# Kernel optimization log

Measured on AMD Instinct MI355X. Metric: run time of the kernel, lower is better.

Reference implementation:

```python
import jax, jax.numpy as jnp
import numpy as np

EPS = 1e-5

def conv(x, w, b, stride, pad):
    y = jax.lax.conv_general_dilated(x, w, (stride, stride), [(pad, pad), (pad, pad)],
                                     dimension_numbers=('NCHW', 'OIHW', 'NCHW'))
    return y + b[None, :, None, None]

def inorm(x):
    # InstanceNorm2d, affine=False, eps=1e-5, biased variance over H,W
    m = x.mean(axis=(2, 3), keepdims=True)
    v = ((x - m) ** 2).mean(axis=(2, 3), keepdims=True)
    return (x - m) * jax.lax.rsqrt(v + EPS)

def setup_inputs() -> dict:
    key = jax.random.key(0)
    ks = jax.random.split(key, 24)
    B = 64
    x = jax.random.normal(ks[0], (B, 5, 256, 192), dtype=jnp.float32)
    chans = [(5, 8), (8, 16), (16, 32), (32, 64), (64, 128), (128, 256)]
    params = {'x': x}
    for i, (ci, co) in enumerate(chans):
        fan = ci * 16
        params[f'w{i}'] = jax.random.normal(ks[1 + 2 * i], (co, ci, 4, 4), jnp.float32) / np.sqrt(fan)
        params[f'b{i}'] = jnp.zeros((co,), jnp.float32)
    for i in (6, 7):
        params[f'w{i}'] = jax.random.normal(ks[1 + 2 * i], (256, 256, 3, 3), jnp.float32) / np.sqrt(256 * 9)
        params[f'b{i}'] = jnp.zeros((256,), jnp.float32)
    params['fc1_w'] = jax.random.normal(ks[20], (128, 512), jnp.float32) / np.sqrt(512)
    params['fc1_b'] = jnp.zeros((128,), jnp.float32)
    # fc2: weight zeroed at init in original; use small random for a nontrivial baseline
    params['fc2_w'] = jax.random.normal(ks[21], (50, 128), jnp.float32) * 0.01
    lin = np.linspace(-0.9, 0.9, 5, dtype=np.float32)
    yy, xx = np.meshgrid(lin, lin, indexing='ij')
    tcp = np.stack([xx.ravel(), yy.ravel()], axis=1)  # [25,2]
    params['fc2_b'] = jnp.asarray(np.arctanh(tcp).reshape(-1))  # [50]
    return params

def reference(x, w0, b0, w1, b1, w2, b2, w3, b3, w4, b4, w5, b5, w6, b6, w7, b7,
              fc1_w, fc1_b, fc2_w, fc2_b):
    B = x.shape[0]
    # block 0: conv -> relu -> instance_norm
    h = inorm(jax.nn.relu(conv(x, w0, b0, 2, 1)))
    # blocks 1..5: conv -> instance_norm -> relu, stride 2
    for w, b in ((w1, b1), (w2, b2), (w3, b3), (w4, b4), (w5, b5)):
        h = jax.nn.relu(inorm(conv(h, w, b, 2, 1)))
    # two 3x3 stride-1 blocks
    for w, b in ((w6, b6), (w7, b7)):
        h = jax.nn.relu(inorm(conv(h, w, b, 1, 1)))
    # maxpool 2x2 stride 2
    h = jax.lax.reduce_window(h, -jnp.inf, jax.lax.max, (1, 1, 2, 2), (1, 1, 2, 2), 'VALID')
    h = h.reshape(B, -1)  # [B,512]
    h = jax.nn.relu(h @ fc1_w.T + fc1_b)
    # F.dropout in eval mode = identity (reference is deterministic)
    pts = jnp.tanh(h @ fc2_w.T + fc2_b)  # [B,50]
    coor = pts.reshape(B, -1, 2)          # [B,25,2]
    grid = coor.reshape(B, 5, 5, 2)       # [B, row j, col i, (x,y)]

    # get_row: squared diffs along i, then abs second difference; stack order (j outer, i inner)
    d_row = (grid[:, :, 1:] - grid[:, :, :-1]) ** 2            # [B,5,4,2]
    row = jnp.abs(d_row[:, :, 1:] - d_row[:, :, :-1]).reshape(B, 15, 2)
    # get_col: same along j; stack order (i outer, j inner)
    gT = jnp.swapaxes(grid, 1, 2)                              # [B, i, j, 2]
    d_col = (gT[:, :, 1:] - gT[:, :, :-1]) ** 2
    col = jnp.abs(d_col[:, :, 1:] - d_col[:, :, :-1]).reshape(B, 15, 2)

    # grad_row / grad_col: curvature cross-product terms, BATCH ELEMENT 0 ONLY (as in original)
    def curv(g):  # g: [5,5,2], triplets along axis 1
        p0, p1, p2 = g[:, :-2], g[:, 1:-1], g[:, 2:]
        x0, y0 = p0[..., 0], p0[..., 1]
        x1, y1 = p1[..., 0], p1[..., 1]
        x2, y2 = p2[..., 0], p2[..., 1]
        return jnp.abs((y1 - y0) * (x1 - x2) - (y1 - y2) * (x1 - x0))  # [5,3]

    g0 = grid[0]
    rg_loss = jnp.maximum(curv(g0).sum(), 0.02)
    cg_loss = jnp.maximum(curv(jnp.swapaxes(g0, 0, 1)).sum(), 0.02)

    rx_loss = jnp.maximum(0.08, row[:, :, 0]).mean()
    ry_loss = jnp.maximum(0.08, row[:, :, 1]).mean()
    cx_loss = jnp.maximum(0.08, col[:, :, 0]).mean()
    cy_loss = jnp.maximum(0.08, col[:, :, 1]).mean()
    return (coor, rx_loss, ry_loss, cx_loss, cy_loss, rg_loss, cg_loss)
```

## Files before the change

### kernel.cpp

```cpp
#include <hip/hip_runtime.h>
#include <hip/hip_bf16.h>
#include <math.h>

#define EPS 1e-5f

__global__ __launch_bounds__(256) void conv0(const float* __restrict__ in,
                                             const float* __restrict__ w,
                                             const float* __restrict__ bias,
                                             float* __restrict__ out)
{
    __shared__ float sW[5 * 8 * 16];
    __shared__ float sB[8];
    int t   = threadIdx.x;
    int n   = blockIdx.x / 24;
    int pxb = blockIdx.x % 24;
    for (int i = t; i < 640; i += 256) {
        int ci = i / 128;
        int r  = i % 128;
        int co = r / 16;
        int k  = r % 16;
        sW[i] = w[((size_t)co * 5 + ci) * 16 + k];
    }
    if (t < 8) sB[t] = bias[t];
    __syncthreads();

    int px0 = (pxb * 256 + t) * 2;
    int oh  = px0 / 96;
    int ow0 = px0 % 96;
    int ih0 = oh * 2 - 1;
    int iwq = ow0 * 2;

    float acc[8][2];
#pragma unroll
    for (int j = 0; j < 8; ++j) { acc[j][0] = sB[j]; acc[j][1] = sB[j]; }

    const float* ib = in + (size_t)n * 5 * 256 * 192;
#pragma unroll 1
    for (int ci = 0; ci < 5; ++ci) {
        const float* plane = ib + (size_t)ci * 256 * 192;
#pragma unroll
        for (int kh = 0; kh < 4; ++kh) {
            int ih = ih0 + kh;
            float p[6];
            if ((unsigned)ih < 256u) {
                const float* row = plane + (size_t)ih * 192;
                float4 q = *(const float4*)(row + iwq);
                p[1] = q.x; p[2] = q.y; p[3] = q.z; p[4] = q.w;
                p[0] = (iwq >= 1)      ? row[iwq - 1] : 0.f;
                p[5] = (iwq + 4 < 192) ? row[iwq + 4] : 0.f;
            } else {
#pragma unroll
                for (int k2 = 0; k2 < 6; ++k2) p[k2] = 0.f;
            }
#pragma unroll
            for (int j = 0; j < 8; ++j) {
                const float4 wv = *(const float4*)(sW + (ci * 8 + j) * 16 + kh * 4);
                acc[j][0] = fmaf(p[0], wv.x, acc[j][0]);
                acc[j][0] = fmaf(p[1], wv.y, acc[j][0]);
                acc[j][0] = fmaf(p[2], wv.z, acc[j][0]);
                acc[j][0] = fmaf(p[3], wv.w, acc[j][0]);
                acc[j][1] = fmaf(p[2], wv.x, acc[j][1]);
                acc[j][1] = fmaf(p[3], wv.y, acc[j][1]);
                acc[j][1] = fmaf(p[4], wv.z, acc[j][1]);
                acc[j][1] = fmaf(p[5], wv.w, acc[j][1]);
            }
        }
    }
    float* ob = out + (size_t)n * 8 * 12288 + px0;
#pragma unroll
    for (int j = 0; j < 8; ++j) {
        float2 v;
        v.x = fmaxf(acc[j][0], 0.f);
        v.y = fmaxf(acc[j][1], 0.f);
        *(float2*)(ob + (size_t)j * 12288) = v;
    }
}

template<int CIN, int CPT>
__global__ void conv42(const float* __restrict__ in, const float* __restrict__ w,
                       const float* __restrict__ bias, float* __restrict__ out,
                       int N, int H, int W, int COUT, int OH, int OW, int relu)
{
    const int NPX = OH * OW;
    const int PXB = NPX / blockDim.x;
    const int NCG = COUT / CPT;

    int bx  = blockIdx.x;
    int pxb = bx % PXB;
    int cg  = (bx / PXB) % NCG;
    int n   = bx / (PXB * NCG);
    int tid = threadIdx.x;

    __shared__ float sW[CPT * CIN * 16];
    for (int i = tid; i < CPT * CIN * 16; i += blockDim.x) {
        int ci = i / (CPT * 16);
        int r  = i % (CPT * 16);
        int j  = r / 16;
        int k  = r % 16;
        sW[i] = w[((size_t)(cg * CPT + j) * CIN + ci) * 16 + k];
    }
    __syncthreads();

    int px = pxb * blockDim.x + tid;
    int oh = px / OW, ow = px % OW;
    int ih0 = oh * 2 - 1, iw0 = ow * 2 - 1;

    float acc[CPT];
#pragma unroll
    for (int j = 0; j < CPT; ++j) acc[j] = bias[cg * CPT + j];

    const float* ib = in + (size_t)n * CIN * H * W;
#pragma unroll 1
    for (int ci = 0; ci < CIN; ++ci) {
        float p[16];
        const float* plane = ib + (size_t)ci * H * W;
#pragma unroll
        for (int kh = 0; kh < 4; ++kh) {
            int ih = ih0 + kh;
            bool vr = (unsigned)ih < (unsigned)H;
            const float* row = plane + (size_t)ih * W;
#pragma unroll
            for (int kw = 0; kw < 4; ++kw) {
                int iw = iw0 + kw;
                bool v = vr && ((unsigned)iw < (unsigned)W);
                p[kh * 4 + kw] = v ? row[iw] : 0.f;
            }
        }
        const float* wp = sW + ci * CPT * 16;
#pragma unroll
        for (int j = 0; j < CPT; ++j) {
            const float* wj = wp + j * 16;
#pragma unroll
            for (int k = 0; k < 16; ++k) acc[j] = fmaf(p[k], wj[k], acc[j]);
        }
    }

#pragma unroll
    for (int j = 0; j < CPT; ++j) {
        float v = acc[j];
        if (relu) v = fmaxf(v, 0.f);
        out[((size_t)(n * COUT + cg * CPT + j) * OH + oh) * OW + ow] = v;
    }
}

__global__ __launch_bounds__(192) void conv_l3s(const float* __restrict__ in,
                                                const float* __restrict__ w,
                                                float* __restrict__ pbuf)
{
    __shared__ float sW[8 * 8 * 16];
    int t  = threadIdx.x;
    int b  = blockIdx.x;
    int cg = b & 7;
    int s  = (b >> 3) & 3;
    int n  = b >> 5;
    for (int i = t; i < 1024; i += 192) {
        int ci = i >> 7;
        int r  = i & 127;
        int j  = r >> 4;
        int k  = r & 15;
        sW[i] = w[((size_t)(cg * 8 + j) * 32 + s * 8 + ci) * 16 + k];
    }
    __syncthreads();

    int oh = t / 12, ow = t % 12;
    int ih0 = oh * 2 - 1, iw0 = ow * 2 - 1;
    float acc[8];
#pragma unroll
    for (int j = 0; j < 8; ++j) acc[j] = 0.f;

    const float* ib = in + ((size_t)n * 32 + s * 8) * 768;
#pragma unroll 1
    for (int ci = 0; ci < 8; ++ci) {
        const float* plane = ib + ci * 768;
        float p[16];
#pragma unroll
        for (int kh = 0; kh < 4; ++kh) {
            int ih = ih0 + kh;
            bool vr = (unsigned)ih < 32u;
#pragma unroll
            for (int kw = 0; kw < 4; ++kw) {
                int iw = iw0 + kw;
                bool v = vr && ((unsigned)iw < 24u);
                p[kh * 4 + kw] = v ? plane[ih * 24 + iw] : 0.f;
            }
        }
        const float* wp = sW + ci * 128;
#pragma unroll
        for (int j = 0; j < 8; ++j) {
#pragma unroll
            for (int k = 0; k < 16; ++k)
                acc[j] = fmaf(p[k], wp[j * 16 + k], acc[j]);
        }
    }
    float* pb = pbuf + (((size_t)s * 64 + n) * 64 + cg * 8) * 192 + t;
#pragma unroll
    for (int j = 0; j < 8; ++j) pb[j * 192] = acc[j];
}

__global__ __launch_bounds__(256) void reduce_norm_l3T(const float* __restrict__ pbuf,
                                                       float* __restrict__ dst_t)
{
    int gid  = blockIdx.x * blockDim.x + threadIdx.x;
    int wv   = gid >> 6;
    int lane = gid & 63;
    int n  = wv >> 6;
    int co = wv & 63;
    float tv[3];
#pragma unroll
    for (int k = 0; k < 3; ++k) {
        int i = lane + k * 64;
        float sum = 0.f;
#pragma unroll
        for (int s = 0; s < 4; ++s)
            sum += pbuf[((size_t)s * 4096 + wv) * 192 + i];
        tv[k] = sum;
    }
    float s1 = tv[0] + tv[1] + tv[2];
    float s2 = tv[0]*tv[0] + tv[1]*tv[1] + tv[2]*tv[2];
    for (int m = 32; m >= 1; m >>= 1) {
        s1 += __shfl_xor(s1, m);
        s2 += __shfl_xor(s2, m);
    }
    float mean = s1 * (1.f / 192.f);
    float var  = s2 * (1.f / 192.f) - mean * mean;
    float r = rsqrtf(var + EPS);
#pragma unroll
    for (int k = 0; k < 3; ++k) {
        int i = lane + k * 64;
        float y = fmaxf((tv[k] - mean) * r, 0.f);
        dst_t[((size_t)co * 192 + i) * 64 + n] = y;
    }
}

template<int TPB, int VPT>
__global__ void inorm_blockv(float* __restrict__ data, int relu)
{
    const int HW = TPB * VPT * 4;
    float4* p = (float4*)(data + (size_t)blockIdx.x * HW);
    float4 v[VPT];
    float s = 0.f, q = 0.f;
#pragma unroll
    for (int k = 0; k < VPT; ++k) {
        v[k] = p[threadIdx.x + k * TPB];
        s += v[k].x + v[k].y + v[k].z + v[k].w;
        q += v[k].x*v[k].x + v[k].y*v[k].y + v[k].z*v[k].z + v[k].w*v[k].w;
    }
    for (int m2 = 32; m2 >= 1; m2 >>= 1) {
        s += __shfl_xor(s, m2);
        q += __shfl_xor(q, m2);
    }
    __shared__ float ss[TPB / 64], sq[TPB / 64], sm[2];
    int wave = threadIdx.x >> 6, lane = threadIdx.x & 63;
    if (lane == 0) { ss[wave] = s; sq[wave] = q; }
    __syncthreads();
    if (threadIdx.x == 0) {
        float a = 0.f, b2 = 0.f;
#pragma unroll
        for (int k = 0; k < TPB / 64; ++k) { a += ss[k]; b2 += sq[k]; }
        float mm = a / (float)HW;
        float vv = b2 / (float)HW - mm * mm;
        sm[0] = mm; sm[1] = rsqrtf(vv + EPS);
    }
    __syncthreads();
    float m = sm[0], r = sm[1];
#pragma unroll
    for (int k = 0; k < VPT; ++k) {
        float4 y;
        y.x = (v[k].x - m) * r; y.y = (v[k].y - m) * r;
        y.z = (v[k].z - m) * r; y.w = (v[k].w - m) * r;
        if (relu) {
            y.x = fmaxf(y.x, 0.f); y.y = fmaxf(y.y, 0.f);
            y.z = fmaxf(y.z, 0.f); y.w = fmaxf(y.w, 0.f);
        }
        p[threadIdx.x + k * TPB] = y;
    }
}

__global__ __launch_bounds__(256) void conv_l4(const float* __restrict__ in_t,
                                               const float* __restrict__ w,
                                               float* __restrict__ pbuf)
{
    int t    = threadIdx.x;
    int lane = t & 63;
    int gw   = __builtin_amdgcn_readfirstlane(blockIdx.x * 4 + (t >> 6));
    int cog  = gw & 63;
    int cic  = (gw >> 6) & 7;
    int half = gw >> 9;
    int cc   = cic * 8;
    int co0  = cog * 2;
    int oh0  = half * 4;

    float acc[2][24];
#pragma unroll
    for (int j = 0; j < 2; ++j)
#pragma unroll
        for (int p = 0; p < 24; ++p) acc[j][p] = 0.f;

    const float* wp = w + ((size_t)co0 * 64 + cc) * 16;

#pragma unroll 1
    for (int ci = 0; ci < 8; ++ci) {
        const float* pl = in_t + (size_t)(cc + ci) * 192 * 64 + lane;
        float wr[2][16];
#pragma unroll
        for (int k = 0; k < 16; ++k) {
            wr[0][k] = wp[(0 * 64 + ci) * 16 + k];
            wr[1][k] = wp[(1 * 64 + ci) * 16 + k];
        }
#pragma unroll
        for (int kh = 0; kh < 4; ++kh) {
            float p[4][12];
#pragma unroll
            for (int o = 0; o < 4; ++o) {
                int ih = 2 * (oh0 + o) - 1 + kh;
                if ((unsigned)ih < 16u) {
#pragma unroll
                    for (int c = 0; c < 12; ++c)
                        p[o][c] = pl[(size_t)(ih * 12 + c) * 64];
                } else {
#pragma unroll
                    for (int c = 0; c < 12; ++c) p[o][c] = 0.f;
                }
            }
#pragma unroll
            for (int o = 0; o < 4; ++o)
#pragma unroll
                for (int ow = 0; ow < 6; ++ow) {
#pragma unroll
                    for (int kw = 0; kw < 4; ++kw) {
                        int iw = 2 * ow - 1 + kw;
                        if (iw < 0 || iw >= 12) continue;
                        float pv = p[o][iw];
                        acc[0][o * 6 + ow] = fmaf(pv, wr[0][kh * 4 + kw], acc[0][o * 6 + ow]);
                        acc[1][o * 6 + ow] = fmaf(pv, wr[1][kh * 4 + kw], acc[1][o * 6 + ow]);
                    }
                }
        }
    }

    float* pb = pbuf + ((size_t)(cic * 64 + lane) * 128 + co0) * 48 + oh0 * 6;
#pragma unroll
    for (int j = 0; j < 2; ++j) {
        float4* o4 = (float4*)(pb + j * 48);
#pragma unroll
        for (int q = 0; q < 6; ++q)
            o4[q] = make_float4(acc[j][q * 4 + 0], acc[j][q * 4 + 1],
                                acc[j][q * 4 + 2], acc[j][q * 4 + 3]);
    }
}

__global__ __launch_bounds__(256) void reduce_norm48(const float* __restrict__ pbuf,
                                                     float* __restrict__ out)
{
    int g  = blockIdx.x * blockDim.x + threadIdx.x;
    int co = g & 127;
    int n  = g >> 7;
    float s[48];
#pragma unroll
    for (int p = 0; p < 48; ++p) s[p] = 0.f;
#pragma unroll 1
    for (int c = 0; c < 8; ++c) {
        const float4* p4 = (const float4*)(pbuf + ((size_t)(c * 64 + n) * 128 + co) * 48);
#pragma unroll
        for (int q = 0; q < 12; ++q) {
            float4 a = p4[q];
            s[q * 4 + 0] += a.x; s[q * 4 + 1] += a.y;
            s[q * 4 + 2] += a.z; s[q * 4 + 3] += a.w;
        }
    }
    float m = 0.f;
#pragma unroll
    for (int p = 0; p < 48; ++p) m += s[p];
    m *= (1.f / 48.f);
    float q = 0.f;
#pragma unroll
    for (int p = 0; p < 48; ++p) { float d = s[p] - m; q += d * d; }
    q *= (1.f / 48.f);
    float r = rsqrtf(q + EPS);
    float4* o4 = (float4*)(out + ((size_t)n * 128 + co) * 48);
#pragma unroll
    for (int qq = 0; qq < 12; ++qq) {
        float4 v;
        v.x = fmaxf((s[qq * 4 + 0] - m) * r, 0.f);
        v.y = fmaxf((s[qq * 4 + 1] - m) * r, 0.f);
        v.z = fmaxf((s[qq * 4 + 2] - m) * r, 0.f);
        v.w = fmaxf((s[qq * 4 + 3] - m) * r, 0.f);
        o4[qq] = v;
    }
}

__global__ __launch_bounds__(256) void conv_l67(const float* __restrict__ in,
                                                const float* __restrict__ w,
                                                float* __restrict__ pbuf)
{
    int t    = threadIdx.x;
    int gw   = __builtin_amdgcn_readfirstlane(blockIdx.x * 4 + (t >> 6));
    int lane = t & 63;
    int cic  = gw >> 6;
    int cog  = gw & 63;
    int cc   = cic * 16;
    int co0  = cog * 4;

    float acc[4][12];
#pragma unroll
    for (int j = 0; j < 4; ++j)
#pragma unroll
        for (int p = 0; p < 12; ++p) acc[j][p] = 0.f;

    const float* ip = in + ((size_t)lane * 256 + cc) * 12;
    const float* wp = w + ((size_t)co0 * 256 + cc) * 9;

#pragma unroll 2
    for (int ci = 0; ci < 16; ++ci) {
        float p[12];
        const float4* p4 = (const float4*)(ip + ci * 12);
        float4 a0 = p4[0], a1 = p4[1], a2 = p4[2];
        p[0] = a0.x; p[1] = a0.y; p[2]  = a0.z; p[3]  = a0.w;
        p[4] = a1.x; p[5] = a1.y; p[6]  = a1.z; p[7]  = a1.w;
        p[8] = a2.x; p[9] = a2.y; p[10] = a2.z; p[11] = a2.w;
#pragma unroll
        for (int j = 0; j < 4; ++j) {
            const float* wj = wp + ((size_t)j * 256 + ci) * 9;
            float wr[9];
#pragma unroll
            for (int k = 0; k < 9; ++k) wr[k] = wj[k];
#pragma unroll
            for (int oh = 0; oh < 4; ++oh)
#pragma unroll
                for (int ow = 0; ow < 3; ++ow)
#pragma unroll
                    for (int kh = 0; kh < 3; ++kh) {
                        int ih = oh - 1 + kh;
                        if (ih < 0 || ih >= 4) continue;
#pragma unroll
                        for (int kw = 0; kw < 3; ++kw) {
                            int iw = ow - 1 + kw;
                            if (iw < 0 || iw >= 3) continue;
                            acc[j][oh * 3 + ow] =
                                fmaf(p[ih * 3 + iw], wr[kh * 3 + kw], acc[j][oh * 3 + ow]);
                        }
                    }
        }
    }

    float* pb = pbuf + ((size_t)(cic * 64 + lane) * 256 + co0) * 12;
#pragma unroll
    for (int j = 0; j < 4; ++j) {
        float4* o4 = (float4*)(pb + j * 12);
        o4[0] = make_float4(acc[j][0], acc[j][1], acc[j][2],  acc[j][3]);
        o4[1] = make_float4(acc[j][4], acc[j][5], acc[j][6],  acc[j][7]);
        o4[2] = make_float4(acc[j][8], acc[j][9], acc[j][10], acc[j][11]);
    }
}

__global__ __launch_bounds__(256) void conv_l5(const float* __restrict__ in,
                                               const float* __restrict__ w,
                                               float* __restrict__ pbuf)
{
    int t    = threadIdx.x;
    int gw   = __builtin_amdgcn_readfirstlane(blockIdx.x * 4 + (t >> 6));
    int lane = t & 63;
    int cic  = gw >> 6;
    int cog  = gw & 63;
    int cc   = cic * 8;
    int co0  = cog * 4;

    float acc[4][12];
#pragma unroll
    for (int j = 0; j < 4; ++j)
#pragma unroll
        for (int p = 0; p < 12; ++p) acc[j][p] = 0.f;

    const float* ip = in + ((size_t)lane * 128 + cc) * 48;
    const float* wp = w + ((size_t)co0 * 128 + cc) * 16;

#pragma unroll 1
    for (int ci = 0; ci < 8; ++ci) {
        float p[48];
        const float4* p4 = (const float4*)(ip + ci * 48);
#pragma unroll
        for (int q = 0; q < 12; ++q) {
            float4 a = p4[q];
            p[q * 4 + 0] = a.x; p[q * 4 + 1] = a.y; p[q * 4 + 2] = a.z; p[q * 4 + 3] = a.w;
        }
#pragma unroll
        for (int j = 0; j < 4; ++j) {
            const float* wj = wp + ((size_t)j * 128 + ci) * 16;
            float wr[16];
#pragma unroll
            for (int k = 0; k < 16; ++k) wr[k] = wj[k];
#pragma unroll
            for (int oh = 0; oh < 4; ++oh)
#pragma unroll
                for (int ow = 0; ow < 3; ++ow) {
                    int ih0 = 2 * oh - 1, iw0 = 2 * ow - 1;
#pragma unroll
                    for (int kh = 0; kh < 4; ++kh) {
                        int ih = ih0 + kh;
                        if (ih < 0 || ih >= 8) continue;
#pragma unroll
                        for (int kw = 0; kw < 4; ++kw) {
                            int iw = iw0 + kw;
                            if (iw < 0 || iw >= 6) continue;
                            acc[j][oh * 3 + ow] =
                                fmaf(p[ih * 6 + iw], wr[kh * 4 + kw], acc[j][oh * 3 + ow]);
                        }
                    }
                }
        }
    }

    float* pb = pbuf + ((size_t)(cic * 64 + lane) * 256 + co0) * 12;
#pragma unroll
    for (int j = 0; j < 4; ++j) {
        float4* o4 = (float4*)(pb + j * 12);
        o4[0] = make_float4(acc[j][0], acc[j][1], acc[j][2],  acc[j][3]);
        o4[1] = make_float4(acc[j][4], acc[j][5], acc[j][6],  acc[j][7]);
        o4[2] = make_float4(acc[j][8], acc[j][9], acc[j][10], acc[j][11]);
    }
}

__global__ __launch_bounds__(256) void reduce_norm12(const float* __restrict__ pbuf,
                                                     float* __restrict__ out)
{
    int g  = blockIdx.x * blockDim.x + threadIdx.x;
    int co = g & 255;
    int n  = g >> 8;
    float s[12];
#pragma unroll
    for (int p = 0; p < 12; ++p) s[p] = 0.f;
#pragma unroll 1
    for (int c = 0; c < 16; ++c) {
        const float4* p4 = (const float4*)(pbuf + ((size_t)(c * 64 + n) * 256 + co) * 12);
        float4 a = p4[0], b = p4[1], d = p4[2];
        s[0] += a.x; s[1] += a.y; s[2]  += a.z; s[3]  += a.w;
        s[4] += b.x; s[5] += b.y; s[6]  += b.z; s[7]  += b.w;
        s[8] += d.x; s[9] += d.y; s[10] += d.z; s[11] += d.w;
    }
    float m = 0.f;
#pragma unroll
    for (int p = 0; p < 12; ++p) m += s[p];
    m *= (1.f / 12.f);
    float q = 0.f;
#pragma unroll
    for (int p = 0; p < 12; ++p) { float d = s[p] - m; q += d * d; }
    q *= (1.f / 12.f);
    float r = rsqrtf(q + EPS);
    float* op = out + ((size_t)n * 256 + co) * 12;
    float4* o4 = (float4*)op;
    float y[12];
#pragma unroll
    for (int p = 0; p < 12; ++p) y[p] = fmaxf((s[p] - m) * r, 0.f);
    o4[0] = make_float4(y[0], y[1], y[2],  y[3]);
    o4[1] = make_float4(y[4], y[5], y[6],  y[7]);
    o4[2] = make_float4(y[8], y[9], y[10], y[11]);
}

__global__ void pool_kernel(const float* __restrict__ in, float* __restrict__ out)
{
    int idx = blockIdx.x * blockDim.x + threadIdx.x;
    if (idx >= 64 * 512) return;
    int f = idx & 511;
    int n = idx >> 9;
    int c = f >> 1;
    int h = f & 1;
    const float* p = in + (((size_t)n * 256 + c) * 4 + h * 2) * 3;
    out[idx] = fmaxf(fmaxf(p[0], p[1]), fmaxf(p[3], p[4]));
}

__global__ void fc1_kernel(const float* __restrict__ in, const float* __restrict__ w,
                           const float* __restrict__ b, float* __restrict__ out)
{
    int idx = blockIdx.x * blockDim.x + threadIdx.x;
    if (idx >= 64 * 128) return;
    int j = idx & 127;
    int n = idx >> 7;
    const float* x  = in + n * 512;
    const float* wr = w + j * 512;
    float acc = b[j];
    for (int f = 0; f < 512; ++f) acc = fmaf(x[f], wr[f], acc);
    out[idx] = fmaxf(acc, 0.f);
}

__global__ void fc2_kernel(const float* __restrict__ in, const float* __restrict__ w,
                           const float* __restrict__ b, float* __restrict__ out)
{
    int idx = blockIdx.x * blockDim.x + threadIdx.x;
    if (idx >= 64 * 50) return;
    int k = idx % 50;
    int n = idx / 50;
    const float* x  = in + n * 128;
    const float* wr = w + k * 128;
    float acc = b[k];
    for (int f = 0; f < 128; ++f) acc = fmaf(x[f], wr[f], acc);
    out[idx] = tanhf(acc);
}

__global__ void loss_kernel(const float* __restrict__ pts, float* __restrict__ out)
{
    __shared__ float acc[4][64];
    int n = threadIdx.x;
    float rx = 0.f, ry = 0.f, cx = 0.f, cy = 0.f;
    {
        const float* g = pts + n * 50;
        for (int r = 0; r < 5; ++r)
            for (int j = 0; j < 3; ++j)
                for (int d = 0; d < 2; ++d) {
                    float a0 = g[(r * 5 + j) * 2 + d];
                    float a1 = g[(r * 5 + j + 1) * 2 + d];
                    float a2 = g[(r * 5 + j + 2) * 2 + d];
                    float d0 = (a1 - a0) * (a1 - a0);
                    float d1 = (a2 - a1) * (a2 - a1);
                    float t = fmaxf(0.08f, fabsf(d1 - d0));
                    if (d == 0) rx += t; else ry += t;
                }
        for (int r = 0; r < 5; ++r)
            for (int j = 0; j < 3; ++j)
                for (int d = 0; d < 2; ++d) {
                    float a0 = g[(j * 5 + r) * 2 + d];
                    float a1 = g[((j + 1) * 5 + r) * 2 + d];
                    float a2 = g[((j + 2) * 5 + r) * 2 + d];
                    float d0 = (a1 - a0) * (a1 - a0);
                    float d1 = (a2 - a1) * (a2 - a1);
                    float t = fmaxf(0.08f, fabsf(d1 - d0));
                    if (d == 0) cx += t; else cy += t;
                }
    }
    acc[0][n] = rx; acc[1][n] = ry; acc[2][n] = cx; acc[3][n] = cy;
    __syncthreads();
    if (n == 0) {
        float s0 = 0.f, s1 = 0.f, s2 = 0.f, s3 = 0.f;
        for (int i = 0; i < 64; ++i) {
            s0 += acc[0][i]; s1 += acc[1][i]; s2 += acc[2][i]; s3 += acc[3][i];
        }
        float inv = 1.0f / (64.0f * 15.0f);
        out[3200] = s0 * inv;
        out[3201] = s1 * inv;
        out[3202] = s2 * inv;
        out[3203] = s3 * inv;
        const float* g = pts;
        float rg = 0.f, cg = 0.f;
        for (int r = 0; r < 5; ++r)
            for (int j = 0; j < 3; ++j) {
                float x0 = g[(r * 5 + j) * 2],     y0 = g[(r * 5 + j) * 2 + 1];
                float x1 = g[(r * 5 + j + 1) * 2], y1 = g[(r * 5 + j + 1) * 2 + 1];
                float x2 = g[(r * 5 + j + 2) * 2], y2 = g[(r * 5 + j + 2) * 2 + 1];
                rg += fabsf((y1 - y0) * (x1 - x2) - (y1 - y2) * (x1 - x0));
            }
        for (int r = 0; r < 5; ++r)
            for (int j = 0; j < 3; ++j) {
                float x0 = g[(j * 5 + r) * 2],       y0 = g[(j * 5 + r) * 2 + 1];
                float x1 = g[((j + 1) * 5 + r) * 2], y1 = g[((j + 1) * 5 + r) * 2 + 1];
                float x2 = g[((j + 2) * 5 + r) * 2], y2 = g[((j + 2) * 5 + r) * 2 + 1];
                cg += fabsf((y1 - y0) * (x1 - x2) - (y1 - y2) * (x1 - x0));
            }
        out[3204] = fmaxf(rg, 0.02f);
        out[3205] = fmaxf(cg, 0.02f);
    }
}

extern "C" void kernel_launch(void* const* d_in, const int* in_sizes, int n_in,
                              void* d_out, int out_size, void* d_ws, size_t ws_size,
                              hipStream_t stream)
{
    const float* x = (const float*)d_in[0];
    const float* w[8], *bia[8];
    for (int i = 0; i < 6; ++i) { w[i] = (const float*)d_in[1 + 2 * i]; bia[i] = (const float*)d_in[2 + 2 * i]; }
    w[6] = (const float*)d_in[13]; bia[6] = (const float*)d_in[14];
    w[7] = (const float*)d_in[15]; bia[7] = (const float*)d_in[16];
    const float* fc1_w = (const float*)d_in[17];
    const float* fc1_b = (const float*)d_in[18];
    const float* fc2_w = (const float*)d_in[19];
    const float* fc2_b = (const float*)d_in[20];
    float* out = (float*)d_out;

    float* A      = (float*)d_ws;
    float* Bf     = A + 6291456;
    float* pooled = Bf + 3145728;
    float* fc1o   = pooled + 32768;
    float* pbuf3  = A + 1572864;
    float* At     = A;
    float* l4out  = A + 1048576;
    float* pbuf   = A + 3145728;

    const int N = 64;

    conv0<<<1536, 256, 0, stream>>>(x, w[0], bia[0], A);
    inorm_blockv<256, 12><<<N * 8, 256, 0, stream>>>(A, 0);

    conv42<8, 8><<<1536, 256, 0, stream>>>(A, w[1], bia[1], Bf, N, 128, 96, 16, 64, 48, 0);
    inorm_blockv<256, 3><<<N * 16, 256, 0, stream>>>(Bf, 1);

    conv42<16, 8><<<768, 256, 0, stream>>>(Bf, w[2], bia[2], A, N, 64, 48, 32, 32, 24, 0);
    inorm_blockv<192, 1><<<N * 32, 192, 0, stream>>>(A, 1);

    conv_l3s<<<2048, 192, 0, stream>>>(A, w[3], pbuf3);
    reduce_norm_l3T<<<1024, 256, 0, stream>>>(pbuf3, At);

    conv_l4<<<256, 256, 0, stream>>>(At, w[4], pbuf);
    reduce_norm48<<<32, 256, 0, stream>>>(pbuf, l4out);

    conv_l5<<<256, 256, 0, stream>>>(l4out, w[5], pbuf);
    reduce_norm12<<<64, 256, 0, stream>>>(pbuf, Bf);

    conv_l67<<<256, 256, 0, stream>>>(Bf, w[6], pbuf);
    reduce_norm12<<<64, 256, 0, stream>>>(pbuf, A);

    conv_l67<<<256, 256, 0, stream>>>(A, w[7], pbuf);
    float* l7out = Bf + 262144;
    reduce_norm12<<<64, 256, 0, stream>>>(pbuf, l7out);

    pool_kernel<<<(64 * 512 + 255) / 256, 256, 0, stream>>>(l7out, pooled);
    fc1_kernel<<<(64 * 128 + 255) / 256, 256, 0, stream>>>(pooled, fc1_w, fc1_b, fc1o);
    fc2_kernel<<<(64 * 50 + 255) / 256, 256, 0, stream>>>(fc1o, fc2_w, fc2_b, out);
    loss_kernel<<<1, 64, 0, stream>>>(out, out);
}
```

Before: 472.9 us.

## Stage conv input tiles with padded halos in shared memory for layers 1-3

Replaces the generic conv42 kernel with conv42L, which loads a zero-padded input tile for a band of output rows into LDS and reads the 4x4 windows from there. conv_l3s gets the same treatment for its whole 32x24 planes. The goal is to drop redundant global loads and per-element bounds checks, since overlapping stride-2 windows re-read each input pixel. The cost is extra LDS use, more syncthreads, and a change from 256- to 192-thread blocks with a different grid size.

After: 574.2 us. +21.4%, slower.

```diff
diff --git a/kernel.cpp b/kernel.cpp
--- a/kernel.cpp
+++ b/kernel.cpp
@@ -76,62 +76,80 @@
     }
 }
 
-template<int CIN, int CPT>
-__global__ void conv42(const float* __restrict__ in, const float* __restrict__ w,
-                       const float* __restrict__ bias, float* __restrict__ out,
-                       int N, int H, int W, int COUT, int OH, int OW, int relu)
-{
-    const int NPX = OH * OW;
-    const int PXB = NPX / blockDim.x;
-    const int NCG = COUT / CPT;
-
+template<int CIN, int CIC, int CPT, int COUT, int H, int W>
+__global__ __launch_bounds__(192) void conv42L(const float* __restrict__ in,
+                                               const float* __restrict__ w,
+                                               const float* __restrict__ bias,
+                                               float* __restrict__ out, int relu)
+{
+    constexpr int OH   = H / 2, OW = W / 2;
+    constexpr int NPX  = OH * OW;
+    constexpr int ROWS = 192 / OW;
+    constexpr int TH   = 2 * ROWS + 2;
+    constexpr int WP   = W + 2;
+    constexpr int NCG  = COUT / CPT;
+    constexpr int PXB  = NPX / 192;
+
+    __shared__ float sT[CIC * TH * WP];
+    __shared__ float sW[CPT * CIC * 16];
+
+    int t   = threadIdx.x;
     int bx  = blockIdx.x;
     int pxb = bx % PXB;
     int cg  = (bx / PXB) % NCG;
     int n   = bx / (PXB * NCG);
-    int tid = threadIdx.x;
-
-    __shared__ float sW[CPT * CIN * 16];
-    for (int i = tid; i < CPT * CIN * 16; i += blockDim.x) {
-        int ci = i / (CPT * 16);
-        int r  = i % (CPT * 16);
-        int j  = r / 16;
-        int k  = r % 16;
-        sW[i] = w[((size_t)(cg * CPT + j) * CIN + ci) * 16 + k];
-    }
-    __syncthreads();
-
-    int px = pxb * blockDim.x + tid;
-    int oh = px / OW, ow = px % OW;
-    int ih0 = oh * 2 - 1, iw0 = ow * 2 - 1;
+
+    int oh0   = pxb * ROWS;
+    int ih_lo = 2 * oh0 - 1;
+
+    int ohl = t / OW;
+    int ow  = t % OW;
+    int oh  = oh0 + ohl;
 
     float acc[CPT];
 #pragma unroll
     for (int j = 0; j < CPT; ++j) acc[j] = bias[cg * CPT + j];
 
-    const float* ib = in + (size_t)n * CIN * H * W;
 #pragma unroll 1
-    for (int ci = 0; ci < CIN; ++ci) {
-        float p[16];
-        const float* plane = ib + (size_t)ci * H * W;
-#pragma unroll
-        for (int kh = 0; kh < 4; ++kh) {
-            int ih = ih0 + kh;
-            bool vr = (unsigned)ih < (unsigned)H;
-            const float* row = plane + (size_t)ih * W;
-#pragma unroll
-            for (int kw = 0; kw < 4; ++kw) {
-                int iw = iw0 + kw;
-                bool v = vr && ((unsigned)iw < (unsigned)W);
-                p[kh * 4 + kw] = v ? row[iw] : 0.f;
+    for (int cc = 0; cc < CIN; cc += CIC) {
+        if (cc) __syncthreads();
+        for (int i = t; i < CIC * TH * WP; i += 192) {
+            int ci  = i / (TH * WP);
+            int r   = i % (TH * WP);
+            int ihp = r / WP;
+            int iwp = r % WP;
+            int ih  = ih_lo + ihp;
+            int iw  = iwp - 1;
+            float v = 0.f;
+            if ((unsigned)ih < (unsigned)H && (unsigned)iw < (unsigned)W)
+                v = in[((size_t)(n * CIN + cc + ci) * H + ih) * W + iw];
+            sT[i] = v;
+        }
+        for (int i = t; i < CPT * CIC * 16; i += 192) {
+            int ci = i / (CPT * 16);
+            int r  = i % (CPT * 16);
+            int j  = r / 16;
+            int k  = r % 16;
+            sW[i] = w[((size_t)(cg * CPT + j) * CIN + cc + ci) * 16 + k];
+        }
+        __syncthreads();
+
+#pragma unroll 1
+        for (int ci = 0; ci < CIC; ++ci) {
+            const float* tp = sT + ci * TH * WP + (2 * ohl) * WP + 2 * ow;
+            float p[16];
+#pragma unroll
+            for (int kh = 0; kh < 4; ++kh)
+#pragma unroll
+                for (int kw = 0; kw < 4; ++kw)
+                    p[kh * 4 + kw] = tp[kh * WP + kw];
+            const float* wp_ = sW + ci * CPT * 16;
+#pragma unroll
+            for (int j = 0; j < CPT; ++j) {
+                const float* wj = wp_ + j * 16;
+#pragma unroll
+                for (int k = 0; k < 16; ++k) acc[j] = fmaf(p[k], wj[k], acc[j]);
             }
-        }
-        const float* wp = sW + ci * CPT * 16;
-#pragma unroll
-        for (int j = 0; j < CPT; ++j) {
-            const float* wj = wp + j * 16;
-#pragma unroll
-            for (int k = 0; k < 16; ++k) acc[j] = fmaf(p[k], wj[k], acc[j]);
         }
     }
 
@@ -147,12 +165,27 @@
                                                 const float* __restrict__ w,
                                                 float* __restrict__ pbuf)
 {
+    __shared__ float sT[8 * 34 * 26];
     __shared__ float sW[8 * 8 * 16];
     int t  = threadIdx.x;
     int b  = blockIdx.x;
     int cg = b & 7;
     int s  = (b >> 3) & 3;
     int n  = b >> 5;
+
+    const float* ib = in + ((size_t)n * 32 + s * 8) * 768;
+    for (int i = t; i < 8 * 884; i += 192) {
+        int ci  = i / 884;
+        int r   = i % 884;
+        int ihp = r / 26;
+        int iwp = r % 26;
+        int ih  = ihp - 1;
+        int iw  = iwp - 1;
+        float v = 0.f;
+        if ((unsigned)ih < 32u && (unsigned)iw < 24u)
+            v = ib[ci * 768 + ih * 24 + iw];
+        sT[i] = v;
+    }
     for (int i = t; i < 1024; i += 192) {
         int ci = i >> 7;
         int r  = i & 127;
@@ -163,27 +196,19 @@
     __syncthreads();
 
     int oh = t / 12, ow = t % 12;
-    int ih0 = oh * 2 - 1, iw0 = ow * 2 - 1;
     float acc[8];
 #pragma unroll
     for (int j = 0; j < 8; ++j) acc[j] = 0.f;
 
-    const float* ib = in + ((size_t)n * 32 + s * 8) * 768;
 #pragma unroll 1
     for (int ci = 0; ci < 8; ++ci) {
-        const float* plane = ib + ci * 768;
+        const float* tp = sT + ci * 884 + (2 * oh) * 26 + 2 * ow;
         float p[16];
 #pragma unroll
-        for (int kh = 0; kh < 4; ++kh) {
-            int ih = ih0 + kh;
-            bool vr = (unsigned)ih < 32u;
-#pragma unroll
-            for (int kw = 0; kw < 4; ++kw) {
-                int iw = iw0 + kw;
-                bool v = vr && ((unsigned)iw < 24u);
-                p[kh * 4 + kw] = v ? plane[ih * 24 + iw] : 0.f;
-            }
-        }
+        for (int kh = 0; kh < 4; ++kh)
+#pragma unroll
+            for (int kw = 0; kw < 4; ++kw)
+                p[kh * 4 + kw] = tp[kh * 26 + kw];
         const float* wp = sW + ci * 128;
 #pragma unroll
         for (int j = 0; j < 8; ++j) {
@@ -688,10 +713,10 @@
     conv0<<<1536, 256, 0, stream>>>(x, w[0], bia[0], A);
     inorm_blockv<256, 12><<<N * 8, 256, 0, stream>>>(A, 0);
 
-    conv42<8, 8><<<1536, 256, 0, stream>>>(A, w[1], bia[1], Bf, N, 128, 96, 16, 64, 48, 0);
+    conv42L<8, 8, 8, 16, 128, 96><<<2048, 192, 0, stream>>>(A, w[1], bia[1], Bf, 0);
     inorm_blockv<256, 3><<<N * 16, 256, 0, stream>>>(Bf, 1);
 
-    conv42<16, 8><<<768, 256, 0, stream>>>(Bf, w[2], bia[2], A, N, 64, 48, 32, 32, 24, 0);
+    conv42L<16, 8, 8, 32, 64, 48><<<1024, 192, 0, stream>>>(Bf, w[2], bia[2], A, 0);
     inorm_blockv<192, 1><<<N * 32, 192, 0, stream>>>(A, 1);
 
     conv_l3s<<<2048, 192, 0, stream>>>(A, w[3], pbuf3);
```
